# Kernel optimization log

Measured on AMD Instinct MI355X. Metric: run time of the kernel, lower is better.

## Reference

```python
import jax, jax.numpy as jnp
import numpy as np

B, N, HID = 4, 1024, 256
NH, DH = 8, 32          # heads, head dim (HID = NH*DH)
BH = 64                 # bias MLP hidden


def setup_inputs() -> dict:
    key = jax.random.key(0)
    ks = jax.random.split(key, 12)
    s = lambda fan_in: 1.0 / np.sqrt(fan_in)
    return {
        "h": jax.random.normal(ks[0], (B, N, HID), jnp.float32),
        "coord": jax.random.uniform(ks[1], (B, N), jnp.float32),
        "mask": jnp.ones((B, N), jnp.int32),
        # qkv / proj linear params (stored [in, out])
        "Wqkv": jax.random.normal(ks[2], (HID, 3 * HID), jnp.float32) * s(HID),
        "bqkv": jnp.zeros((3 * HID,), jnp.float32),
        "Wproj": jax.random.normal(ks[3], (HID, HID), jnp.float32) * s(HID),
        "bproj": jnp.zeros((HID,), jnp.float32),
        # layernorm
        "gamma": jnp.ones((HID,), jnp.float32),
        "beta": jnp.zeros((HID,), jnp.float32),
        # relative-bias MLP: Linear(1->BH), SiLU, Linear(BH->BH), SiLU, Linear(BH->NH)
        "Wb1": jax.random.normal(ks[4], (1, BH), jnp.float32),
        "bb1": jnp.zeros((BH,), jnp.float32),
        "Wb2": jax.random.normal(ks[5], (BH, BH), jnp.float32) * s(BH),
        "bb2": jnp.zeros((BH,), jnp.float32),
        "Wb3": jax.random.normal(ks[6], (BH, NH), jnp.float32) * s(BH),
        "bb3": jnp.zeros((NH,), jnp.float32),
    }


def _layernorm(x, gamma, beta, eps=1e-5):
    mu = jnp.mean(x, axis=-1, keepdims=True)
    var = jnp.mean((x - mu) ** 2, axis=-1, keepdims=True)
    return (x - mu) * jax.lax.rsqrt(var + eps) * gamma + beta


def reference(h, coord, mask, Wqkv, bqkv, Wproj, bproj, gamma, beta,
              Wb1, bb1, Wb2, bb2, Wb3, bb3):
    x = _layernorm(h, gamma, beta)                      # [B,N,HID]
    qkv = x @ Wqkv + bqkv                               # [B,N,3*HID]
    q, k, v = jnp.split(qkv, 3, axis=-1)
    # [B,N,HID] -> [B,NH,N,DH]
    reshape = lambda t: t.reshape(B, N, NH, DH).transpose(0, 2, 1, 3)
    q, k, v = reshape(q), reshape(k), reshape(v)

    attn = jnp.einsum("bhqd,bhkd->bhqk", q, k) / np.sqrt(DH).astype(np.float32)

    # pairwise coordinate differences and learned bias
    dcoord = coord[:, None, :] - coord[:, :, None]      # [B,N,N]
    t = dcoord[..., None]                               # [B,N,N,1]
    t = jax.nn.silu(t @ Wb1 + bb1)                      # [B,N,N,BH]
    t = jax.nn.silu(t @ Wb2 + bb2)                      # [B,N,N,BH]
    bias = (t @ Wb3 + bb3)                              # [B,N,N,NH]
    attn = attn + bias.transpose(0, 3, 1, 2)            # [B,NH,N,N]

    neg_inf = jnp.array(-jnp.inf, attn.dtype)
    attn = jnp.where(mask[:, None, None, :] == 0, neg_inf, attn)
    w = jax.nn.softmax(attn, axis=-1)

    out = jnp.einsum("bhqk,bhkd->bhqd", w, v)           # [B,NH,N,DH]
    out = out.transpose(0, 2, 1, 3).reshape(B, N, HID)
    out = out @ Wproj + bproj
    return h + out
```

## Files before the change

### kernel.cpp

```cpp
#include <hip/hip_runtime.h>
#include <hip/hip_fp16.h>
#include <math.h>

#define BB   4
#define NN   1024
#define HIDD 256
#define NHD  8
#define DHD  32
#define BHD  64
#define TI4  4096
#define TBS  4104
#define NSPL 2
#define LOG2E 1.4426950408889634f

typedef __attribute__((ext_vector_type(8))) short bf16x8;
typedef __attribute__((ext_vector_type(4))) short bf16x4;
typedef __attribute__((ext_vector_type(4))) float f32x4;

__device__ __forceinline__ unsigned short f2bf(float x) {
  union { float f; unsigned u; } c; c.f = x;
  unsigned r = c.u + 0x7FFFu + ((c.u >> 16) & 1u);
  return (unsigned short)(r >> 16);
}
__device__ __forceinline__ float bf2f(unsigned short b) {
  union { unsigned u; float f; } c; c.u = ((unsigned)b) << 16;
  return c.f;
}

__device__ __forceinline__ void pv_mfma(f32x4& acc, bf16x4 a, bf16x4 b) {
#if __has_builtin(__builtin_amdgcn_mfma_f32_16x16x16bf16_1k)
  acc = __builtin_amdgcn_mfma_f32_16x16x16bf16_1k(a, b, acc, 0, 0, 0);
#else
  asm volatile("s_nop 1\n\t"
               "v_mfma_f32_16x16x16_bf16 %0, %1, %2, %0\n\t"
               "s_nop 7\n\t"
               "s_nop 3"
               : "+v"(acc) : "v"(a), "v"(b));
#endif
}

__global__ __launch_bounds__(256) void prep_kernel(
    const float* __restrict__ Wb1, const float* __restrict__ bb1,
    const float* __restrict__ Wb2, const float* __restrict__ bb2,
    const float* __restrict__ Wb3, const float* __restrict__ bb3,
    const float* __restrict__ Wqkv, const float* __restrict__ Wproj,
    unsigned short* __restrict__ tblb, unsigned short* __restrict__ wtq,
    unsigned short* __restrict__ wtp)
{
  __shared__ float h1a[4][64], h2a[4][64];
  __shared__ float t[16][17];
  int bid = blockIdx.x, tid = threadIdx.x;
  if (bid < 1025) {
    int g = tid >> 6, j = tid & 63;
    int pt = bid * 4 + g;
    float tt = -1.0f + (float)pt * (2.0f / (float)TI4);
    float z0 = fmaf(tt, Wb1[j], bb1[j]);
    h1a[g][j] = z0 / (1.0f + __expf(-z0));
    __syncthreads();
    float a0 = bb2[j];
    #pragma unroll 16
    for (int i = 0; i < BHD; ++i) a0 = fmaf(h1a[g][i], Wb2[i*BHD + j], a0);
    h2a[g][j] = a0 / (1.0f + __expf(-a0));
    __syncthreads();
    if (j < NHD && pt <= TI4) {
      float o0 = bb3[j];
      #pragma unroll 16
      for (int i = 0; i < BHD; ++i) o0 = fmaf(h2a[g][i], Wb3[i*NHD + j], o0);
      tblb[j*TBS + pt] = f2bf(o0 * LOG2E);
    }
  } else {
    const float* W; unsigned short* Wt; int n0, k0, ncols;
    if (bid < 1793) {
      int rb = bid - 1025;
      n0 = (rb % 48) * 16; k0 = (rb / 48) * 16; ncols = 768;
      W = Wqkv; Wt = wtq;
    } else {
      int rc = bid - 1793;
      n0 = (rc & 15) * 16; k0 = (rc >> 4) * 16; ncols = 256;
      W = Wproj; Wt = wtp;
    }
    int sx = tid & 15, sy = tid >> 4;
    t[sy][sx] = W[(size_t)(k0 + sy) * ncols + n0 + sx];
    __syncthreads();
    Wt[(size_t)(n0 + sy) * 256 + k0 + sx] = f2bf(t[sx][sy]);
  }
}

__global__ __launch_bounds__(256) void ln_qkv_mm_kernel(
    const float* __restrict__ h, const float* __restrict__ gamma,
    const float* __restrict__ beta, const unsigned short* __restrict__ Wt,
    const float* __restrict__ bqkv,
    unsigned short* __restrict__ qws, unsigned short* __restrict__ kws,
    unsigned short* __restrict__ vtws)
{
  __shared__ unsigned short xs[16][260];
  int tid = threadIdx.x;
  int m0 = blockIdx.x * 16, n0 = blockIdx.y * 128;

  {
    int r = tid >> 4, q = tid & 15;
    const float* hrow = h + (size_t)(m0 + r)*HIDD + q*16;
    float4 xv[4];
    float sum = 0.f, sq = 0.f;
    #pragma unroll
    for (int j = 0; j < 4; ++j) {
      xv[j] = *(const float4*)&hrow[j*4];
      sum += xv[j].x + xv[j].y + xv[j].z + xv[j].w;
      sq  += xv[j].x*xv[j].x + xv[j].y*xv[j].y + xv[j].z*xv[j].z + xv[j].w*xv[j].w;
    }
    sum += __shfl_xor(sum, 1); sq += __shfl_xor(sq, 1);
    sum += __shfl_xor(sum, 2); sq += __shfl_xor(sq, 2);
    sum += __shfl_xor(sum, 4); sq += __shfl_xor(sq, 4);
    sum += __shfl_xor(sum, 8); sq += __shfl_xor(sq, 8);
    float mu  = sum * (1.0f/HIDD);
    float var = sq  * (1.0f/HIDD) - mu*mu;
    float rs  = rsqrtf(var + 1e-5f);
    #pragma unroll
    for (int j2 = 0; j2 < 2; ++j2) {
      union { bf16x8 v; unsigned short u[8]; } o;
      #pragma unroll
      for (int e = 0; e < 2; ++e) {
        float4 x4 = xv[j2*2 + e];
        int col = q*16 + j2*8 + e*4;
        float4 gv = *(const float4*)&gamma[col];
        float4 bv = *(const float4*)&beta[col];
        o.u[e*4+0] = f2bf(fmaf((x4.x - mu)*rs, gv.x, bv.x));
        o.u[e*4+1] = f2bf(fmaf((x4.y - mu)*rs, gv.y, bv.y));
        o.u[e*4+2] = f2bf(fmaf((x4.z - mu)*rs, gv.z, bv.z));
        o.u[e*4+3] = f2bf(fmaf((x4.w - mu)*rs, gv.w, bv.w));
      }
      *(bf16x8*)&xs[r][q*16 + j2*8] = o.v;
    }
  }
  __syncthreads();

  int lane = tid & 63, w = tid >> 6;
  int lo = lane & 15, hi = lane >> 4;
  int cw = w * 32;
  f32x4 acc[2];
  acc[0] = (f32x4){0.f,0.f,0.f,0.f};
  acc[1] = (f32x4){0.f,0.f,0.f,0.f};

  #pragma unroll
  for (int ks = 0; ks < 8; ++ks) {
    bf16x8 af = *(const bf16x8*)&xs[lo][ks*32 + hi*8];
    #pragma unroll
    for (int nt = 0; nt < 2; ++nt) {
      bf16x8 bf = *(const bf16x8*)&Wt[(size_t)(n0 + cw + nt*16 + lo)*256 + ks*32 + hi*8];
      acc[nt] = __builtin_amdgcn_mfma_f32_16x16x32_bf16(af, bf, acc[nt], 0, 0, 0);
    }
  }

  int b = m0 >> 10;
  if (n0 < 512) {
    unsigned short* dst = (n0 < 256) ? qws : kws;
    int nbase = (m0 & 1023) + hi*4;
    #pragma unroll
    for (int nt = 0; nt < 2; ++nt) {
      int c = n0 + cw + nt*16 + lo;
      int cr = c & 255;
      int head = cr >> 5, d = cr & 31;
      float bq = bqkv[c];
      size_t bh = (size_t)(b*NHD + head);
      #pragma unroll
      for (int r = 0; r < 4; ++r)
        dst[(bh*NN + nbase + r)*DHD + d] = f2bf(acc[nt][r] + bq);
    }
  } else {
    __syncthreads();
    unsigned short (*vt)[20] = (unsigned short(*)[20])&xs[0][0];
    #pragma unroll
    for (int nt = 0; nt < 2; ++nt) {
      int cr = cw + nt*16 + lo;
      float bq = bqkv[n0 + cr];
      union { unsigned short u[4]; unsigned wd[2]; } pk;
      #pragma unroll
      for (int r = 0; r < 4; ++r) pk.u[r] = f2bf(acc[nt][r] + bq);
      int col = hi*4;
      *(unsigned*)&vt[cr][col]     = pk.wd[0];
      *(unsigned*)&vt[cr][col + 2] = pk.wd[1];
    }
    __syncthreads();
    int nn0 = m0 & 1023;
    int row = tid >> 1, ch = tid & 1;
    int cr256 = (n0 - 512) + row;
    int head = cr256 >> 5, d = cr256 & 31;
    *(bf16x8*)&vtws[((size_t)(b*NHD + head)*DHD + d)*NN + nn0 + ch*8] =
        *(const bf16x8*)&vt[row][ch*8];
  }
}

__global__ __launch_bounds__(256, 4) void attn_kernel(
    const unsigned short* __restrict__ Q, const unsigned short* __restrict__ K,
    const unsigned short* __restrict__ Vt, const float* __restrict__ coord,
    const int* __restrict__ mask, const unsigned short* __restrict__ tblb,
    unsigned short* __restrict__ pO, float2* __restrict__ pML)
{
  __shared__ unsigned short tableL[TBS];
  __shared__ unsigned short Klds[2][64][40];
  __shared__ unsigned short Vtlds[2][32][72];
  __shared__ __align__(16) float ckL[NN/NSPL];
  __shared__ __align__(16) int   mkL[NN/NSPL];

  int tid = threadIdx.x, lane = tid & 63, w = tid >> 6;
  int bh = blockIdx.y, half = blockIdx.z;
  int b = bh >> 3, head = bh & 7;
  int qbase = blockIdx.x * 64 + w * 16;
  int lo = lane & 15, hi = lane >> 4;

  {
    const uint4* src = (const uint4*)(tblb + head*TBS);
    uint4* dst = (uint4*)tableL;
    for (int i = tid; i < TBS/8; i += 256) dst[i] = src[i];
  }

  bf16x8 qf = *(const bf16x8*)&Q[((size_t)bh*NN + qbase + lo)*DHD + hi*8];
  float qoff2 = fmaf(coord[b*NN + qbase + lo], -(float)TI4*0.5f, (float)TI4*0.5f);

  float m = -1e30f, l = 0.f;
  f32x4 oacc[2];
  oacc[0] = (f32x4){0.f,0.f,0.f,0.f};
  oacc[1] = (f32x4){0.f,0.f,0.f,0.f};
  const float scale2 = 0.17677669529663689f * LOG2E;

  int kt0 = half * (NN/NSPL);
  int sr = tid >> 2, ss = tid & 3;
  int vr = tid >> 3, vs = tid & 7;
  {
    #pragma unroll
    for (int i = 0; i < (NN/NSPL)/256; ++i) {
      int idx = i*256 + tid;
      ckL[idx] = coord[b*NN + kt0 + idx];
      mkL[idx] = mask [b*NN + kt0 + idx];
    }
    *(bf16x8*)&Klds[0][sr][ss*8] =
        *(const bf16x8*)&K[((size_t)bh*NN + kt0 + sr)*DHD + ss*8];
    *(bf16x8*)&Vtlds[0][vr][vs*8] =
        *(const bf16x8*)&Vt[((size_t)bh*DHD + vr)*NN + kt0 + vs*8];
  }
  __syncthreads();

  for (int t = 0; t < NN/NSPL/64; ++t) {
    int kt = kt0 + t*64;
    int cur = t & 1;
    bf16x8 kn, vn;
    if (t < NN/NSPL/64 - 1) {
      kn = *(const bf16x8*)&K[((size_t)bh*NN + kt + 64 + sr)*DHD + ss*8];
      vn = *(const bf16x8*)&Vt[((size_t)bh*DHD + vr)*NN + kt + 64 + vs*8];
    }
    float ck[4][4]; int mk[4][4];
    #pragma unroll
    for (int nt = 0; nt < 4; ++nt) {
      float4 c4 = *(const float4*)&ckL[t*64 + nt*16 + hi*4];
      int4   m4 = *(const int4*)  &mkL[t*64 + nt*16 + hi*4];
      ck[nt][0] = c4.x; ck[nt][1] = c4.y; ck[nt][2] = c4.z; ck[nt][3] = c4.w;
      mk[nt][0] = m4.x; mk[nt][1] = m4.y; mk[nt][2] = m4.z; mk[nt][3] = m4.w;
    }

    f32x4 z = {0.f,0.f,0.f,0.f};
    f32x4 sacc[4];
    #pragma unroll
    for (int nt = 0; nt < 4; ++nt) {
      bf16x8 kf = *(const bf16x8*)&Klds[cur][nt*16 + lo][hi*8];
      sacc[nt] = __builtin_amdgcn_mfma_f32_16x16x32_bf16(kf, qf, z, 0, 0, 0);
    }

    float sv[4][4];
    #pragma unroll
    for (int nt = 0; nt < 4; ++nt) {
      #pragma unroll
      for (int r = 0; r < 4; ++r) {
        float u = fmaf(ck[nt][r], (float)TI4*0.5f, qoff2);
        int i0 = (int)(u + 0.5f);
        float bias = bf2f(tableL[i0]);
        float s = fmaf(sacc[nt][r], scale2, bias);
        sv[nt][r] = mk[nt][r] ? s : -1e31f;
      }
    }

    float pm = sv[0][0];
    #pragma unroll
    for (int nt = 0; nt < 4; ++nt)
      #pragma unroll
      for (int r = 0; r < 4; ++r) pm = fmaxf(pm, sv[nt][r]);
    pm = fmaxf(pm, __shfl_xor(pm, 16));
    pm = fmaxf(pm, __shfl_xor(pm, 32));
    if (!__all(pm <= m + 8.0f)) {
      float mn = fmaxf(m, pm);
      float sf = __builtin_amdgcn_exp2f(m - mn);
      l *= sf;
      #pragma unroll
      for (int n2 = 0; n2 < 2; ++n2)
        #pragma unroll
        for (int r = 0; r < 4; ++r) oacc[n2][r] *= sf;
      m = mn;
    }

    bf16x4 pfrag[4];
    #pragma unroll
    for (int nt = 0; nt < 4; ++nt) {
      float p0 = __builtin_amdgcn_exp2f(sv[nt][0] - m);
      float p1 = __builtin_amdgcn_exp2f(sv[nt][1] - m);
      float p2 = __builtin_amdgcn_exp2f(sv[nt][2] - m);
      float p3 = __builtin_amdgcn_exp2f(sv[nt][3] - m);
      l += (p0 + p1) + (p2 + p3);
      union { bf16x4 v; unsigned short u[4]; } pk;
      pk.u[0] = f2bf(p0); pk.u[1] = f2bf(p1);
      pk.u[2] = f2bf(p2); pk.u[3] = f2bf(p3);
      pfrag[nt] = pk.v;
    }

    #pragma unroll
    for (int nt = 0; nt < 4; ++nt) {
      #pragma unroll
      for (int n2 = 0; n2 < 2; ++n2) {
        bf16x4 vf = *(const bf16x4*)&Vtlds[cur][n2*16 + lo][nt*16 + hi*4];
        pv_mfma(oacc[n2], vf, pfrag[nt]);
      }
    }

    if (t < NN/NSPL/64 - 1) {
      *(bf16x8*)&Klds[cur^1][sr][ss*8] = kn;
      *(bf16x8*)&Vtlds[cur^1][vr][vs*8] = vn;
    }
    __syncthreads();
  }

  l += __shfl_xor(l, 16);
  l += __shfl_xor(l, 32);
  size_t base = ((size_t)(half*BB*NHD + bh)*NN + qbase + lo);
  #pragma unroll
  for (int n2 = 0; n2 < 2; ++n2) {
    union { bf16x4 v; unsigned short u[4]; } ov;
    ov.u[0] = f2bf(oacc[n2][0]); ov.u[1] = f2bf(oacc[n2][1]);
    ov.u[2] = f2bf(oacc[n2][2]); ov.u[3] = f2bf(oacc[n2][3]);
    *(bf16x4*)&pO[base*DHD + n2*16 + hi*4] = ov.v;
  }
  if (hi == 0) pML[base] = make_float2(m, l);
}

__global__ __launch_bounds__(256) void proj_mm_kernel(
    const unsigned short* __restrict__ pO, const float2* __restrict__ pML,
    const unsigned short* __restrict__ Wpt, const float* __restrict__ bp,
    const float* __restrict__ h, float* __restrict__ out)
{
  __shared__ unsigned short alds[32][264];
  int tid = threadIdx.x;
  int m0 = blockIdx.x * 32, n0 = blockIdx.y * 32;

  {
    int r = tid >> 3, q = tid & 7;
    int g = m0 + r, b = g >> 10, n = g & 1023;
    int bhh = b*NHD + q;
    float2 ml0 = pML[(size_t)bhh*NN + n];
    float2 ml1 = pML[((size_t)(BB*NHD) + bhh)*NN + n];
    float mm = fmaxf(ml0.x, ml1.x);
    float e0 = __builtin_amdgcn_exp2f(ml0.x - mm);
    float e1 = __builtin_amdgcn_exp2f(ml1.x - mm);
    float inv = 1.0f / fmaf(ml0.y, e0, ml1.y * e1);
    e0 *= inv; e1 *= inv;
    const bf16x8* p0 = (const bf16x8*)&pO[((size_t)bhh*NN + n)*DHD];
    const bf16x8* p1 = (const bf16x8*)&pO[(((size_t)(BB*NHD) + bhh)*NN + n)*DHD];
    #pragma unroll
    for (int j = 0; j < 4; ++j) {
      union { bf16x8 v; unsigned short u[8]; } a, c, o;
      a.v = p0[j]; c.v = p1[j];
      #pragma unroll
      for (int e = 0; e < 8; ++e)
        o.u[e] = f2bf(fmaf(bf2f(a.u[e]), e0, bf2f(c.u[e]) * e1));
      *(bf16x8*)&alds[r][q*32 + j*8] = o.v;
    }
  }
  __syncthreads();

  int lane = tid & 63, w = tid >> 6;
  int lo = lane & 15, hi = lane >> 4;
  int mw = (w & 1) * 16;
  int nw = n0 + (w >> 1) * 16;
  f32x4 acc = (f32x4){0.f,0.f,0.f,0.f};

  #pragma unroll
  for (int ks = 0; ks < 8; ++ks) {
    bf16x8 af = *(const bf16x8*)&alds[mw + lo][ks*32 + hi*8];
    bf16x8 bf = *(const bf16x8*)&Wpt[(size_t)(nw + lo)*256 + ks*32 + hi*8];
    acc = __builtin_amdgcn_mfma_f32_16x16x32_bf16(af, bf, acc, 0, 0, 0);
  }

  int c = nw + lo;
  float bpv = bp[c];
  #pragma unroll
  for (int r = 0; r < 4; ++r) {
    size_t o = (size_t)(m0 + mw + hi*4 + r)*HIDD + c;
    out[o] = h[o] + acc[r] + bpv;
  }
}

extern "C" void kernel_launch(void* const* d_in, const int* in_sizes, int n_in,
                              void* d_out, int out_size, void* d_ws, size_t ws_size,
                              hipStream_t stream)
{
  const float* h     = (const float*)d_in[0];
  const float* coord = (const float*)d_in[1];
  const int*   mask  = (const int*)  d_in[2];
  const float* Wqkv  = (const float*)d_in[3];
  const float* bqkv  = (const float*)d_in[4];
  const float* Wproj = (const float*)d_in[5];
  const float* bproj = (const float*)d_in[6];
  const float* gamma = (const float*)d_in[7];
  const float* beta  = (const float*)d_in[8];
  const float* Wb1   = (const float*)d_in[9];
  const float* bb1   = (const float*)d_in[10];
  const float* Wb2   = (const float*)d_in[11];
  const float* bb2   = (const float*)d_in[12];
  const float* Wb3   = (const float*)d_in[13];
  const float* bb3   = (const float*)d_in[14];
  float* out = (float*)d_out;

  unsigned short* tblb = (unsigned short*)d_ws;
  float2* pML = (float2*)(tblb + NHD*TBS);
  unsigned short* wtq  = (unsigned short*)(pML + (size_t)NSPL*BB*NHD*NN);
  unsigned short* wtp  = wtq + 768*256;
  unsigned short* qws  = wtp + 256*256;
  unsigned short* kws  = qws + (size_t)BB*NHD*NN*DHD;
  unsigned short* vtws = kws + (size_t)BB*NHD*NN*DHD;
  unsigned short* pO   = vtws + (size_t)BB*NHD*NN*DHD;

  prep_kernel<<<dim3(2049), dim3(256), 0, stream>>>(
      Wb1, bb1, Wb2, bb2, Wb3, bb3, Wqkv, Wproj, tblb, wtq, wtp);
  ln_qkv_mm_kernel<<<dim3(BB*NN/16, 6), dim3(256), 0, stream>>>(
      h, gamma, beta, wtq, bqkv, qws, kws, vtws);
  attn_kernel<<<dim3(NN/64, BB*NHD, NSPL), dim3(256), 0, stream>>>(
      qws, kws, vtws, coord, mask, tblb, pO, pML);
  proj_mm_kernel<<<dim3(BB*NN/32, HIDD/32), dim3(256), 0, stream>>>(
      pO, pML, wtp, bproj, h, out);
}
```

Baseline: 64.27 us.

## Halve bias table resolution and fold key mask into table sentinel lookup

Halves the number of precomputed bias-table points and extends each head's table with a region filled with a large negative value. Masked keys get a sentinel coordinate that indexes into that region, so the per-element mask load and select in the attention loop are removed. The bias table also gets smaller, which cuts prep-kernel work and shared memory. Halving the table resolution makes the nearest-neighbour bias lookup coarser and may lower accuracy.

```diff
diff --git a/kernel.cpp b/kernel.cpp
--- a/kernel.cpp
+++ b/kernel.cpp
@@ -1,5 +1,6 @@
 #include <hip/hip_runtime.h>
 #include <hip/hip_fp16.h>
+#include <hip/hip_bf16.h>
 #include <math.h>
 
 #define BB   4
@@ -8,8 +9,8 @@
 #define NHD  8
 #define DHD  32
 #define BHD  64
-#define TI4  4096
-#define TBS  4104
+#define TI2  2048
+#define TBSX 3592
 #define NSPL 2
 #define LOG2E 1.4426950408889634f
 
@@ -18,9 +19,9 @@
 typedef __attribute__((ext_vector_type(4))) float f32x4;
 
 __device__ __forceinline__ unsigned short f2bf(float x) {
-  union { float f; unsigned u; } c; c.f = x;
-  unsigned r = c.u + 0x7FFFu + ((c.u >> 16) & 1u);
-  return (unsigned short)(r >> 16);
+  union { __hip_bfloat16 h; unsigned short u; } c;
+  c.h = __float2bfloat16(x);
+  return c.u;
 }
 __device__ __forceinline__ float bf2f(unsigned short b) {
   union { unsigned u; float f; } c; c.u = ((unsigned)b) << 16;
@@ -50,10 +51,10 @@
   __shared__ float h1a[4][64], h2a[4][64];
   __shared__ float t[16][17];
   int bid = blockIdx.x, tid = threadIdx.x;
-  if (bid < 1025) {
+  if (bid < 513) {
     int g = tid >> 6, j = tid & 63;
     int pt = bid * 4 + g;
-    float tt = -1.0f + (float)pt * (2.0f / (float)TI4);
+    float tt = -1.0f + (float)pt * (2.0f / (float)TI2);
     float z0 = fmaf(tt, Wb1[j], bb1[j]);
     h1a[g][j] = z0 / (1.0f + __expf(-z0));
     __syncthreads();
@@ -62,20 +63,25 @@
     for (int i = 0; i < BHD; ++i) a0 = fmaf(h1a[g][i], Wb2[i*BHD + j], a0);
     h2a[g][j] = a0 / (1.0f + __expf(-a0));
     __syncthreads();
-    if (j < NHD && pt <= TI4) {
+    if (j < NHD && pt <= TI2) {
       float o0 = bb3[j];
       #pragma unroll 16
       for (int i = 0; i < BHD; ++i) o0 = fmaf(h2a[g][i], Wb3[i*NHD + j], o0);
-      tblb[j*TBS + pt] = f2bf(o0 * LOG2E);
-    }
+      tblb[j*TBSX + pt] = f2bf(o0 * LOG2E);
+    }
+  } else if (bid < 521) {
+    int head = bid - 513;
+    unsigned short neg = f2bf(-1e31f);
+    for (int i = tid; i < TBSX - (TI2 + 1); i += 256)
+      tblb[head*TBSX + TI2 + 1 + i] = neg;
   } else {
     const float* W; unsigned short* Wt; int n0, k0, ncols;
-    if (bid < 1793) {
-      int rb = bid - 1025;
+    if (bid < 1289) {
+      int rb = bid - 521;
       n0 = (rb % 48) * 16; k0 = (rb / 48) * 16; ncols = 768;
       W = Wqkv; Wt = wtq;
     } else {
-      int rc = bid - 1793;
+      int rc = bid - 1289;
       n0 = (rc & 15) * 16; k0 = (rc >> 4) * 16; ncols = 256;
       W = Wproj; Wt = wtp;
     }
@@ -196,11 +202,10 @@
     const int* __restrict__ mask, const unsigned short* __restrict__ tblb,
     unsigned short* __restrict__ pO, float2* __restrict__ pML)
 {
-  __shared__ unsigned short tableL[TBS];
+  __shared__ unsigned short tableL[TBSX];
   __shared__ unsigned short Klds[2][64][40];
   __shared__ unsigned short Vtlds[2][32][72];
   __shared__ __align__(16) float ckL[NN/NSPL];
-  __shared__ __align__(16) int   mkL[NN/NSPL];
 
   int tid = threadIdx.x, lane = tid & 63, w = tid >> 6;
   int bh = blockIdx.y, half = blockIdx.z;
@@ -209,13 +214,13 @@
   int lo = lane & 15, hi = lane >> 4;
 
   {
-    const uint4* src = (const uint4*)(tblb + head*TBS);
+    const uint4* src = (const uint4*)(tblb + head*TBSX);
     uint4* dst = (uint4*)tableL;
-    for (int i = tid; i < TBS/8; i += 256) dst[i] = src[i];
+    for (int i = tid; i < TBSX/8; i += 256) dst[i] = src[i];
   }
 
   bf16x8 qf = *(const bf16x8*)&Q[((size_t)bh*NN + qbase + lo)*DHD + hi*8];
-  float qoff2 = fmaf(coord[b*NN + qbase + lo], -(float)TI4*0.5f, (float)TI4*0.5f);
+  float qoff2 = fmaf(coord[b*NN + qbase + lo], -(float)TI2*0.5f, (float)TI2*0.5f);
 
   float m = -1e30f, l = 0.f;
   f32x4 oacc[2];
@@ -230,8 +235,7 @@
     #pragma unroll
     for (int i = 0; i < (NN/NSPL)/256; ++i) {
       int idx = i*256 + tid;
-      ckL[idx] = coord[b*NN + kt0 + idx];
-      mkL[idx] = mask [b*NN + kt0 + idx];
+      ckL[idx] = mask[b*NN + kt0 + idx] ? coord[b*NN + kt0 + idx] : 2.5f;
     }
     *(bf16x8*)&Klds[0][sr][ss*8] =
         *(const bf16x8*)&K[((size_t)bh*NN + kt0 + sr)*DHD + ss*8];
@@ -248,13 +252,11 @@
       kn = *(const bf16x8*)&K[((size_t)bh*NN + kt + 64 + sr)*DHD + ss*8];
       vn = *(const bf16x8*)&Vt[((size_t)bh*DHD + vr)*NN + kt + 64 + vs*8];
     }
-    float ck[4][4]; int mk[4][4];
+    float ck[4][4];
     #pragma unroll
     for (int nt = 0; nt < 4; ++nt) {
       float4 c4 = *(const float4*)&ckL[t*64 + nt*16 + hi*4];
-      int4   m4 = *(const int4*)  &mkL[t*64 + nt*16 + hi*4];
       ck[nt][0] = c4.x; ck[nt][1] = c4.y; ck[nt][2] = c4.z; ck[nt][3] = c4.w;
-      mk[nt][0] = m4.x; mk[nt][1] = m4.y; mk[nt][2] = m4.z; mk[nt][3] = m4.w;
     }
 
     f32x4 z = {0.f,0.f,0.f,0.f};
@@ -270,11 +272,9 @@
     for (int nt = 0; nt < 4; ++nt) {
       #pragma unroll
       for (int r = 0; r < 4; ++r) {
-        float u = fmaf(ck[nt][r], (float)TI4*0.5f, qoff2);
+        float u = fmaf(ck[nt][r], (float)TI2*0.5f, qoff2);
         int i0 = (int)(u + 0.5f);
-        float bias = bf2f(tableL[i0]);
-        float s = fmaf(sacc[nt][r], scale2, bias);
-        sv[nt][r] = mk[nt][r] ? s : -1e31f;
+        sv[nt][r] = fmaf(sacc[nt][r], scale2, bf2f(tableL[i0]));
       }
     }
 
@@ -417,7 +417,7 @@
   float* out = (float*)d_out;
 
   unsigned short* tblb = (unsigned short*)d_ws;
-  float2* pML = (float2*)(tblb + NHD*TBS);
+  float2* pML = (float2*)(tblb + NHD*TBSX + 4);
   unsigned short* wtq  = (unsigned short*)(pML + (size_t)NSPL*BB*NHD*NN);
   unsigned short* wtp  = wtq + 768*256;
   unsigned short* qws  = wtp + 256*256;
@@ -425,7 +425,7 @@
   unsigned short* vtws = kws + (size_t)BB*NHD*NN*DHD;
   unsigned short* pO   = vtws + (size_t)BB*NHD*NN*DHD;
 
-  prep_kernel<<<dim3(2049), dim3(256), 0, stream>>>(
+  prep_kernel<<<dim3(1545), dim3(256), 0, stream>>>(
       Wb1, bb1, Wb2, bb2, Wb3, bb3, Wqkv, Wproj, tblb, wtq, wtp);
   ln_qkv_mm_kernel<<<dim3(BB*NN/16, 6), dim3(256), 0, stream>>>(
       h, gamma, beta, wtq, bqkv, qws, kws, vtws);
```

Result: faster. 61.62 us (-4.1%).
